# Kernel tuning notes

Hardware: AMD Instinct MI355X
Metric: run time of the kernel (lower is better)

## Reference

```python
import jax, jax.numpy as jnp
import numpy as np

B, P, N, E = 32, 1024, 1024, 128
HQ = 128  # head_num * qkv_dim == embedding_dim
SQRT_E = 11.313708498984761
LOGIT_CLIP = 10.0


def setup_inputs() -> dict:
    key = jax.random.key(0)
    ks = jax.random.split(key, 16)
    s = 1.0 / np.sqrt(E)
    return {
        "encoded_nodes": jax.random.normal(ks[0], (B, N, E), jnp.float32),
        "encoded_q1": jax.random.normal(ks[1], (B, P, E), jnp.float32),
        "encoded_q2": jax.random.normal(ks[2], (B, P, E), jnp.float32),
        "encoded_last_node": jax.random.normal(ks[3], (B, P, E), jnp.float32),
        "load": jax.random.uniform(ks[4], (B, P), jnp.float32),
        "left": jax.random.uniform(ks[5], (B, P), jnp.float32),
        "cur_dist": jax.random.uniform(ks[6], (B, P, N), jnp.float32),
        "log_scale": jnp.ones((), jnp.float32),
        "ninf_mask": jnp.zeros((B, P, N), jnp.float32),
        "Wq1": jax.random.normal(ks[7], (E, HQ), jnp.float32) * s,
        "Wq2": jax.random.normal(ks[8], (E, HQ), jnp.float32) * s,
        "Wq_last": jax.random.normal(ks[9], (E + 2, HQ), jnp.float32) * s,
        "Wk": jax.random.normal(ks[10], (E, HQ), jnp.float32) * s,
        "Wv": jax.random.normal(ks[11], (E, HQ), jnp.float32) * s,
        "AFT_dist_alpha": jnp.ones((1,), jnp.float32),
        "probs_dist_alpha": jnp.ones((1,), jnp.float32),
    }


def reference(encoded_nodes, encoded_q1, encoded_q2, encoded_last_node, load, left,
              cur_dist, log_scale, ninf_mask, Wq1, Wq2, Wq_last, Wk, Wv,
              AFT_dist_alpha, probs_dist_alpha):
    # set_kv / set_q1 / set_q2
    k = encoded_nodes @ Wk                      # [B,N,HQ]
    v = encoded_nodes @ Wv                      # [B,N,HQ]
    single_head_key = jnp.swapaxes(encoded_nodes, 1, 2)  # [B,E,N]
    q1 = encoded_q1 @ Wq1                       # [B,P,HQ]
    q2 = encoded_q2 @ Wq2

    input_cat = jnp.concatenate([encoded_last_node, load[:, :, None], left[:, :, None]], axis=2)
    q_last = input_cat @ Wq_last                # [B,P,HQ]
    q = q1 + q2 + q_last

    cur_dist_out = -cur_dist                    # [B,P,N]
    sigmoid_q = jax.nn.sigmoid(q)
    bias_scale = log_scale * AFT_dist_alpha[0] * cur_dist_out + ninf_mask
    e_bias = jnp.exp(bias_scale)                # [B,P,N]
    ek = jnp.exp(k)                             # [B,N,HQ]
    num = jnp.nan_to_num(jnp.einsum('bpn,bnd->bpd', e_bias, ek * v))
    den = jnp.nan_to_num(jnp.einsum('bpn,bnd->bpd', e_bias, ek)) + 1e-20
    AFT_out = sigmoid_q * (num / den)           # [B,P,HQ]

    score = jnp.einsum('bpd,bdn->bpn', AFT_out, single_head_key)
    score_scaled = score / SQRT_E + log_scale * probs_dist_alpha[0] * cur_dist_out
    score_clipped = LOGIT_CLIP * jnp.tanh(score_scaled)
    probs = jax.nn.softmax(score_clipped + ninf_mask, axis=2)
    return probs
```

## Files before the change

### kernel.cpp

```cpp
#include <hip/hip_runtime.h>
#include <math.h>

#define Bb 32
#define Pp 1024
#define Nn 1024

typedef unsigned short u16;
typedef __bf16 bf16x8 __attribute__((ext_vector_type(8)));
typedef float f32x4 __attribute__((ext_vector_type(4)));
typedef u16 us8 __attribute__((ext_vector_type(8)));
typedef u16 us4 __attribute__((ext_vector_type(4)));

#define MFMA __builtin_amdgcn_mfma_f32_16x16x32_bf16

static constexpr float INV_SQRT_E = 0.08838834764831845f;

__device__ __forceinline__ bf16x8 asbf(us8 v) { return __builtin_bit_cast(bf16x8, v); }

__device__ __forceinline__ void bsplit(float x, u16& h, u16& l) {
  unsigned u = __float_as_uint(x);
  unsigned r = u + 0x7FFF + ((u >> 16) & 1);
  h = (u16)(r >> 16);
  float hf = __uint_as_float((unsigned)h << 16);
  float lof = x - hf;
  unsigned u2 = __float_as_uint(lof);
  unsigned r2 = u2 + 0x7FFF + ((u2 >> 16) & 1);
  l = (u16)(r2 >> 16);
}

__device__ __forceinline__ void tsplit(float x, u16& h, u16& l) {
  unsigned u = __float_as_uint(x);
  h = (u16)(u >> 16);
  float lof = x - __uint_as_float(u & 0xFFFF0000u);
  l = (u16)(__float_as_uint(lof) >> 16);
}

__device__ __forceinline__ float exp10tanh(float s) {
  float ax = fabsf(s);
  float u = __expf(-2.0f * ax);
  float r = __builtin_amdgcn_rcpf(1.0f + u);
  float tt = fmaf(-2.0f * u, r, 1.0f);
  tt = copysignf(tt, s);
  return __expf(10.0f * tt);
}

__global__ __launch_bounds__(256) void prep_weights(
    const float* __restrict__ Wq1, const float* __restrict__ Wq2,
    const float* __restrict__ Wql, const float* __restrict__ Wk,
    const float* __restrict__ Wv, u16* __restrict__ wcat_hi, u16* __restrict__ wcat_lo,
    u16* __restrict__ wkv_hi, u16* __restrict__ wkv_lo) {
  int t = threadIdx.x;
  if (blockIdx.x == 0) {
    for (int i = t; i < 128 * 384; i += 256) {
      int c = i / 384, k = i % 384;
      float v = (k < 128) ? Wq1[k * 128 + c]
                          : (k < 256) ? Wq2[(k - 128) * 128 + c] : Wql[(k - 256) * 128 + c];
      u16 h, l;
      bsplit(v, h, l);
      wcat_hi[i] = h;
      wcat_lo[i] = l;
    }
  } else {
    for (int i = t; i < 256 * 128; i += 256) {
      int c = i >> 7, k = i & 127;
      float v = (c < 128) ? Wk[k * 128 + c] : Wv[k * 128 + (c - 128)];
      u16 h, l;
      bsplit(v, h, l);
      wkv_hi[i] = h;
      wkv_lo[i] = l;
    }
  }
}

__global__ __launch_bounds__(256, 1) void kv_prep(
    const float* __restrict__ nodes, const u16* __restrict__ wkv_hi,
    const u16* __restrict__ wkv_lo, u16* __restrict__ ekkP_hi, u16* __restrict__ ekkP_lo,
    u16* __restrict__ nodesP_hi, u16* __restrict__ nodesP_lo) {
  __shared__ u16 a_hi[32 * 136], a_lo[32 * 136];
  __shared__ float kvbuf[32 * 264];
  const int t = threadIdx.x;
  const int xcd = blockIdx.x & 7, jj = blockIdx.x >> 3;
  const int b = xcd * 4 + (jj >> 5);
  const int n0 = (jj & 31) * 32;
  for (int i = t; i < 4096; i += 256) {
    int n = i >> 7, d = i & 127;
    float v = nodes[((long)(b * 1024 + n0 + n)) * 128 + d];
    u16 h, l;
    bsplit(v, h, l);
    a_hi[n * 136 + d] = h;
    a_lo[n * 136 + d] = l;
  }
  __syncthreads();
  const int lane = t & 63, w = t >> 6;
  const int lr = lane & 15, lg = lane >> 4;
  f32x4 acc0[2][4] = {}, acc1[2][4] = {};
#pragma unroll
  for (int ks = 0; ks < 4; ++ks) {
    us8 ah[2], al[2];
#pragma unroll
    for (int mt = 0; mt < 2; ++mt) {
      int ro = (lr + 16 * mt) * 136 + ks * 32 + lg * 8;
      ah[mt] = *(const us8*)&a_hi[ro];
      al[mt] = *(const us8*)&a_lo[ro];
    }
    us8 bh[4], bl[4];
#pragma unroll
    for (int cc = 0; cc < 4; ++cc) {
      long off = (long)((w * 4 + cc) * 16 + lr) * 128 + ks * 32 + lg * 8;
      bh[cc] = *(const us8*)&wkv_hi[off];
      bl[cc] = *(const us8*)&wkv_lo[off];
    }
#pragma unroll
    for (int mt = 0; mt < 2; ++mt)
#pragma unroll
      for (int cc = 0; cc < 4; ++cc) {
        acc0[mt][cc] = MFMA(asbf(ah[mt]), asbf(bh[cc]), acc0[mt][cc], 0, 0, 0);
        acc1[mt][cc] = MFMA(asbf(al[mt]), asbf(bh[cc]), acc1[mt][cc], 0, 0, 0);
        acc1[mt][cc] = MFMA(asbf(ah[mt]), asbf(bl[cc]), acc1[mt][cc], 0, 0, 0);
      }
  }
#pragma unroll
  for (int mt = 0; mt < 2; ++mt)
#pragma unroll
    for (int cc = 0; cc < 4; ++cc) {
      int c = (w * 4 + cc) * 16 + lr;
#pragma unroll
      for (int r = 0; r < 4; ++r)
        kvbuf[(lg * 4 + r + 16 * mt) * 264 + c] = acc0[mt][cc][r] + acc1[mt][cc][r];
    }
  __syncthreads();
#pragma unroll
  for (int jo = 0; jo < 4; ++jo) {
    int c = jo * 64 + (t & 63);
    int i4 = t >> 6;
    int kcol = (c < 128) ? c : (c - 128);
    us8 h8, l8;
#pragma unroll
    for (int jq = 0; jq < 8; ++jq) {
      int n = i4 * 8 + jq;
      float kv = kvbuf[n * 264 + kcol];
      float ek = __expf(kv);
      float val = (c < 128) ? ek * kvbuf[n * 264 + c + 128] : ek;
      u16 h, l;
      bsplit(val, h, l);
      h8[jq] = h;
      l8[jq] = l;
    }
    long o = (((long)b * 128 + (n0 >> 3) + i4) * 256 + c) * 8;
    *(us8*)&ekkP_hi[o] = h8;
    *(us8*)&ekkP_lo[o] = l8;
  }
  {
    int pl = t >> 7, r = t & 127;
    int dgrp = r >> 3, nb = r & 7;
    const u16* src = pl ? a_lo : a_hi;
    u16* dst = pl ? nodesP_lo : nodesP_hi;
#pragma unroll
    for (int i = 0; i < 4; ++i) {
      int n = nb + 8 * i;
      us8 v = *(const us8*)&src[n * 136 + dgrp * 8];
      *(us8*)&dst[(((long)(b * 16 + dgrp)) * 1024 + n0 + n) * 8] = v;
    }
  }
}

__global__ __launch_bounds__(256) void qsig_prep(
    const float* __restrict__ q1m, const float* __restrict__ q2m,
    const float* __restrict__ lnm, const float* __restrict__ loadv,
    const float* __restrict__ leftv, const float* __restrict__ Wql,
    const u16* __restrict__ wcat_hi, const u16* __restrict__ wcat_lo,
    float* __restrict__ qsig) {
  const int t = threadIdx.x;
  const int lane = t & 63, w = t >> 6;
  const int lr = lane & 15, lg = lane >> 4;
  const long p0 = (long)blockIdx.x * 16;
  const long arow = p0 + lr;
  f32x4 qacc[2] = {};
#pragma unroll 2
  for (int s = 0; s < 12; ++s) {
    const float* __restrict__ src = (s < 4) ? q1m : (s < 8) ? q2m : lnm;
    long ao = arow * 128 + (s & 3) * 32 + lg * 8;
    float4 a0 = *(const float4*)&src[ao];
    float4 a1 = *(const float4*)&src[ao + 4];
    float av[8] = {a0.x, a0.y, a0.z, a0.w, a1.x, a1.y, a1.z, a1.w};
    us8 ah, al;
#pragma unroll
    for (int jq = 0; jq < 8; ++jq) {
      u16 hh, ll;
      tsplit(av[jq], hh, ll);
      ah[jq] = hh;
      al[jq] = ll;
    }
#pragma unroll
    for (int cf = 0; cf < 2; ++cf) {
      int c = w * 32 + cf * 16 + lr;
      us8 bh = *(const us8*)&wcat_hi[c * 384 + s * 32 + lg * 8];
      us8 bl = *(const us8*)&wcat_lo[c * 384 + s * 32 + lg * 8];
      qacc[cf] = MFMA(asbf(ah), asbf(bh), qacc[cf], 0, 0, 0);
      qacc[cf] = MFMA(asbf(al), asbf(bh), qacc[cf], 0, 0, 0);
      qacc[cf] = MFMA(asbf(ah), asbf(bl), qacc[cf], 0, 0, 0);
    }
  }
#pragma unroll
  for (int cf = 0; cf < 2; ++cf) {
    int c = w * 32 + cf * 16 + lr;
    float wl1 = Wql[128 * 128 + c], wl2 = Wql[129 * 128 + c];
#pragma unroll
    for (int r = 0; r < 4; ++r) {
      int row = lg * 4 + r;
      float qv = qacc[cf][r] + loadv[p0 + row] * wl1 + leftv[p0 + row] * wl2;
      qsig[(p0 + row) * 128 + c] = 1.0f / (1.0f + __expf(-qv));
    }
  }
}

struct DFset {
  float4 d0, d1, f0, f1;
};

__global__ __launch_bounds__(512, 2) void ndaft_gemm(
    const float* __restrict__ cdist, const float* __restrict__ ninf,
    const u16* __restrict__ ekkP_hi, const u16* __restrict__ ekkP_lo,
    const float* __restrict__ qsig, u16* __restrict__ aftP_hi,
    u16* __restrict__ aftP_lo, u16* __restrict__ bias16,
    const float* __restrict__ logs, const float* __restrict__ aal,
    const float* __restrict__ pal) {
  __shared__ u16 lds[25088];
  const int t = threadIdx.x;
  const int lane = t & 63, w = t >> 6;
  const int lr = lane & 15, lg = lane >> 4;
  const int wr = w >> 2, wc = w & 3;
  const int xcd = blockIdx.x & 7, j = blockIdx.x >> 3;
  const int b = xcd * 4 + (j & 3);
  const int pt = j >> 2;
  const long bp = (long)b * Pp + pt * 128;
  const float c1 = logs[0] * aal[0];
  const float c2 = logs[0] * pal[0];

  const int srow = t >> 2, soct = t & 3;
  const long arow = bp + srow;
  const long tbase = (arow >> 4) * 32768;
  const int spr = srow & 15, sptile = srow >> 4;
  const long bsrc = (long)b * 128 * 2048;

  DFset dfA, dfB;
  us8 bst[4];
  us8 ebh, ebl;

  auto load_df = [&](DFset& df, int s) {
    long ao = arow * 1024 + s * 32 + soct * 8;
    df.d0 = *(const float4*)&cdist[ao];
    df.d1 = *(const float4*)&cdist[ao + 4];
    df.f0 = *(const float4*)&ninf[ao];
    df.f1 = *(const float4*)&ninf[ao + 4];
  };
  auto load_bst = [&](int s) {
    long sb = bsrc + (long)s * 8192;
#pragma unroll
    for (int i = 0; i < 2; ++i) {
      bst[i] = *(const us8*)&ekkP_hi[sb + (i * 512 + t) * 8];
      bst[i + 2] = *(const us8*)&ekkP_lo[sb + (i * 512 + t) * 8];
    }
  };
  auto compute_eb = [&](DFset& df, int s) {
    float dv[8] = {df.d0.x, df.d0.y, df.d0.z, df.d0.w, df.d1.x, df.d1.y, df.d1.z, df.d1.w};
    float nv[8] = {df.f0.x, df.f0.y, df.f0.z, df.f0.w, df.f1.x, df.f1.y, df.f1.z, df.f1.w};
    us8 q8;
#pragma unroll
    for (int jq = 0; jq < 8; ++jq) {
      float e = __expf(fmaf(-c1, dv[jq], nv[jq]));
      u16 h, l;
      tsplit(e, h, l);
      ebh[jq] = h;
      ebl[jq] = l;
      float x = fminf(fmaxf(c2 * dv[jq], 0.f), 15.999f);
      q8[jq] = (nv[jq] < -1e5f) ? (u16)0xFFFF : (u16)(x * 4096.f + 0.5f);
    }
    *(us8*)&bias16[tbase + ((s * 4 + soct) * 16 + spr) * 8] = q8;
  };
  auto write_lds = [&]() {
    *(us8*)&lds[((sptile * 2 + 0) * 4 + soct) * 136 + spr * 8] = ebh;
    *(us8*)&lds[((sptile * 2 + 1) * 4 + soct) * 136 + spr * 8] = ebl;
#pragma unroll
    for (int i = 0; i < 2; ++i) {
      *(us8*)&lds[8704 + (i * 512 + t) * 8] = bst[i];
      *(us8*)&lds[8704 + 8192 + (i * 512 + t) * 8] = bst[i + 2];
    }
  };

  f32x4 acc[4][4] = {};

  load_df(dfA, 0);
  load_df(dfB, 1);
  load_bst(0);
  compute_eb(dfA, 0);

  auto stage = [&](int s, DFset& refill, DFset& consume) {
    asm volatile("s_waitcnt lgkmcnt(0)" ::: "memory");
    __builtin_amdgcn_s_barrier();
    __builtin_amdgcn_sched_barrier(0);
    write_lds();
    asm volatile("s_waitcnt lgkmcnt(0)" ::: "memory");
    __builtin_amdgcn_s_barrier();
    __builtin_amdgcn_sched_barrier(0);
    if (s < 31) load_bst(s + 1);
    if (s < 30) load_df(refill, s + 2);
    if (s < 31) compute_eb(consume, s + 1);
    us8 ah[4], al[4];
#pragma unroll
    for (int mt = 0; mt < 4; ++mt) {
      int ptl = wr * 4 + mt;
      ah[mt] = *(const us8*)&lds[((ptl * 2 + 0) * 4 + lg) * 136 + lr * 8];
      al[mt] = *(const us8*)&lds[((ptl * 2 + 1) * 4 + lg) * 136 + lr * 8];
    }
#pragma unroll
    for (int ct = 0; ct < 4; ++ct) {
      int c = (ct < 2) ? (wc * 32 + ct * 16 + lr) : (96 + wc * 32 + ct * 16 + lr);
      us8 bh = *(const us8*)&lds[8704 + lg * 2048 + c * 8];
      us8 bl = *(const us8*)&lds[8704 + 8192 + lg * 2048 + c * 8];
#pragma unroll
      for (int mt = 0; mt < 4; ++mt) {
        acc[mt][ct] = MFMA(asbf(ah[mt]), asbf(bh), acc[mt][ct], 0, 0, 0);
        acc[mt][ct] = MFMA(asbf(al[mt]), asbf(bh), acc[mt][ct], 0, 0, 0);
        acc[mt][ct] = MFMA(asbf(ah[mt]), asbf(bl), acc[mt][ct], 0, 0, 0);
      }
    }
  };

#pragma unroll 1
  for (int s2 = 0; s2 < 32; s2 += 2) {
    stage(s2, dfA, dfB);
    stage(s2 + 1, dfB, dfA);
  }

#pragma unroll
  for (int mt = 0; mt < 4; ++mt)
#pragma unroll
    for (int ct = 0; ct < 2; ++ct) {
      int cn = wc * 32 + ct * 16 + lr;
      int nc = cn >> 3, jq = cn & 7;
#pragma unroll
      for (int r = 0; r < 4; ++r) {
        long gr = bp + wr * 64 + mt * 16 + lg * 4 + r;
        float sig = qsig[gr * 128 + cn];
        float aftv = sig * acc[mt][ct][r] * __builtin_amdgcn_rcpf(acc[mt][ct + 2][r] + 1e-20f);
        u16 h, l;
        bsplit(aftv, h, l);
        long idx = (gr >> 4) * 2048 + (nc * 16 + (gr & 15)) * 8 + jq;
        aftP_hi[idx] = h;
        aftP_lo[idx] = l;
      }
    }
}

__global__ __launch_bounds__(256, 4) void score_softmax(
    const u16* bias16, const u16* __restrict__ aftP_hi, const u16* __restrict__ aftP_lo,
    const u16* __restrict__ nodesP_hi, const u16* __restrict__ nodesP_lo,
    float* out) {
  __shared__ float psum[16 * 4];
  __shared__ float invb[16];
  const int t = threadIdx.x;
  const int lane = t & 63, w = t >> 6;
  const int lr = lane & 15, lg = lane >> 4;
  const int xcd = blockIdx.x & 7, j = blockIdx.x >> 3;
  const int b = xcd * 4 + (j >> 6);
  const int tl = j & 63;
  const int p0 = tl * 16;
  const long bp = (long)b * Pp + p0;
  const int tile = b * 64 + tl;

  f32x4 sacc[16] = {};
#pragma unroll
  for (int ks = 0; ks < 4; ++ks) {
    long aoff = (long)tile * 2048 + ((long)((ks * 4 + lg) * 16 + lr)) * 8;
    us8 ah = *(const us8*)&aftP_hi[aoff];
    us8 al = *(const us8*)&aftP_lo[aoff];
    long nb = ((long)(b * 16 + ks * 4 + lg)) * 1024;
    auto bld = [&](int cf, us8& bh, us8& bl) {
      long o = (nb + w * 256 + cf * 16 + lr) * 8;
      bh = *(const us8*)&nodesP_hi[o];
      bl = *(const us8*)&nodesP_lo[o];
    };
    us8 bh0, bl0, bh1, bl1;
    bld(0, bh0, bl0);
    bld(1, bh1, bl1);
#pragma unroll
    for (int cf = 0; cf < 16; ++cf) {
      us8 nh = bh1, nl = bl1;
      if (cf < 14) bld(cf + 2, nh, nl);
      sacc[cf] = MFMA(asbf(bh0), asbf(ah), sacc[cf], 0, 0, 0);
      sacc[cf] = MFMA(asbf(bl0), asbf(ah), sacc[cf], 0, 0, 0);
      sacc[cf] = MFMA(asbf(bh0), asbf(al), sacc[cf], 0, 0, 0);
      bh0 = bh1; bl0 = bl1; bh1 = nh; bl1 = nl;
    }
  }

  const long btile = (long)tile * 32768;
  float rs = 0.f;
#pragma unroll
  for (int cf = 0; cf < 16; ++cf) {
    int nc = w * 32 + cf * 2 + (lg >> 1);
    int j0 = (lg & 1) * 4;
    us4 q4 = *(const us4*)&bias16[btile + (nc * 16 + lr) * 8 + j0];
#pragma unroll
    for (int r = 0; r < 4; ++r) {
      u16 qv = q4[r];
      float sv = fmaf(sacc[cf][r], INV_SQRT_E, (float)qv * -2.44140625e-4f);
      float e = exp10tanh(sv);
      e = (qv == (u16)0xFFFF) ? 0.f : e;
      sacc[cf][r] = e;
      rs += e;
    }
  }
  rs += __shfl_xor(rs, 16);
  rs += __shfl_xor(rs, 32);
  if (lane < 16) psum[lr * 4 + w] = rs;
  __syncthreads();
  if (t < 16)
    invb[t] = 1.0f / (psum[t * 4] + psum[t * 4 + 1] + psum[t * 4 + 2] + psum[t * 4 + 3]);
  __syncthreads();

  const float inv = invb[lr];
  const long ro = (bp + lr) * (long)Nn + w * 256;
#pragma unroll
  for (int cf = 0; cf < 16; ++cf) {
    float4 v;
    v.x = sacc[cf][0] * inv;
    v.y = sacc[cf][1] * inv;
    v.z = sacc[cf][2] * inv;
    v.w = sacc[cf][3] * inv;
    *(float4*)&out[ro + cf * 16 + lg * 4] = v;
  }
}

extern "C" void kernel_launch(void* const* d_in, const int* in_sizes, int n_in,
                              void* d_out, int out_size, void* d_ws, size_t ws_size,
                              hipStream_t stream) {
  const float* nodes = (const float*)d_in[0];
  const float* q1m = (const float*)d_in[1];
  const float* q2m = (const float*)d_in[2];
  const float* lnm = (const float*)d_in[3];
  const float* loadv = (const float*)d_in[4];
  const float* leftv = (const float*)d_in[5];
  const float* cdist = (const float*)d_in[6];
  const float* logs = (const float*)d_in[7];
  const float* ninf = (const float*)d_in[8];
  const float* Wq1 = (const float*)d_in[9];
  const float* Wq2 = (const float*)d_in[10];
  const float* Wql = (const float*)d_in[11];
  const float* Wk = (const float*)d_in[12];
  const float* Wv = (const float*)d_in[13];
  const float* aalpha = (const float*)d_in[14];
  const float* palpha = (const float*)d_in[15];

  char* ws = (char*)d_ws;
  u16* ekkP_hi = (u16*)ws;
  u16* ekkP_lo = (u16*)(ws + (16ul << 20));
  u16* nodesP_hi = (u16*)(ws + (32ul << 20));
  u16* nodesP_lo = (u16*)(ws + (40ul << 20));
  float* qsig = (float*)(ws + (48ul << 20));
  u16* aftP_hi = (u16*)(ws + (64ul << 20));
  u16* aftP_lo = (u16*)(ws + (72ul << 20));
  u16* wcat_hi = (u16*)(ws + (80ul << 20));
  u16* wcat_lo = wcat_hi + 128 * 384;
  u16* wkv_hi = wcat_lo + 128 * 384;
  u16* wkv_lo = wkv_hi + 256 * 128;
  u16* bias16 = (u16*)d_out;

  prep_weights<<<2, 256, 0, stream>>>(Wq1, Wq2, Wql, Wk, Wv, wcat_hi, wcat_lo, wkv_hi, wkv_lo);
  kv_prep<<<Bb * Nn / 32, 256, 0, stream>>>(nodes, wkv_hi, wkv_lo, ekkP_hi, ekkP_lo,
                                            nodesP_hi, nodesP_lo);
  qsig_prep<<<2048, 256, 0, stream>>>(q1m, q2m, lnm, loadv, leftv, Wql, wcat_hi, wcat_lo,
                                      qsig);
  ndaft_gemm<<<256, 512, 0, stream>>>(cdist, ninf, ekkP_hi, ekkP_lo, qsig, aftP_hi,
                                      aftP_lo, bias16, logs, aalpha, palpha);
  score_softmax<<<Bb * Pp / 16, 256, 0, stream>>>(
      bias16, aftP_hi, aftP_lo, nodesP_hi, nodesP_lo, (float*)d_out);
}
```

Baseline: 349.3 us.

## Load B operand directly to registers and double-buffer A tile in LDS

The ek/ekv B-operand fragments are now loaded straight from global memory into registers in MFMA layout, instead of being staged through LDS. The A tile (exp bias split into hi/lo) is double-buffered in LDS, which drops one of the two barriers per k-step. The aim is less LDS traffic and less barrier stalling in the main GEMM loop. The cost is more VGPRs for two sets of B registers and redundant global reads of B, since each wave fetches its own columns.

New measurement: 359.9 us. +3.0%, slower.

```diff
diff --git a/kernel.cpp b/kernel.cpp
--- a/kernel.cpp
+++ b/kernel.cpp
@@ -225,7 +225,7 @@
     u16* __restrict__ aftP_lo, u16* __restrict__ bias16,
     const float* __restrict__ logs, const float* __restrict__ aal,
     const float* __restrict__ pal) {
-  __shared__ u16 lds[25088];
+  __shared__ u16 lds[2][8704];
   const int t = threadIdx.x;
   const int lane = t & 63, w = t >> 6;
   const int lr = lane & 15, lg = lane >> 4;
@@ -243,8 +243,12 @@
   const int spr = srow & 15, sptile = srow >> 4;
   const long bsrc = (long)b * 128 * 2048;
 
+  int ccol[4];
+#pragma unroll
+  for (int ct = 0; ct < 4; ++ct)
+    ccol[ct] = (ct < 2) ? (wc * 32 + ct * 16 + lr) : (96 + wc * 32 + ct * 16 + lr);
+
   DFset dfA, dfB;
-  us8 bst[4];
   us8 ebh, ebl;
 
   auto load_df = [&](DFset& df, int s) {
@@ -254,12 +258,12 @@
     df.f0 = *(const float4*)&ninf[ao];
     df.f1 = *(const float4*)&ninf[ao + 4];
   };
-  auto load_bst = [&](int s) {
-    long sb = bsrc + (long)s * 8192;
-#pragma unroll
-    for (int i = 0; i < 2; ++i) {
-      bst[i] = *(const us8*)&ekkP_hi[sb + (i * 512 + t) * 8];
-      bst[i + 2] = *(const us8*)&ekkP_lo[sb + (i * 512 + t) * 8];
+  auto load_B = [&](int s, us8 (&bh)[4], us8 (&bl)[4]) {
+    long sb = bsrc + (long)s * 8192 + (long)lg * 2048;
+#pragma unroll
+    for (int ct = 0; ct < 4; ++ct) {
+      bh[ct] = *(const us8*)&ekkP_hi[sb + ccol[ct] * 8];
+      bl[ct] = *(const us8*)&ekkP_lo[sb + ccol[ct] * 8];
     }
   };
   auto compute_eb = [&](DFset& df, int s) {
@@ -278,59 +282,57 @@
     }
     *(us8*)&bias16[tbase + ((s * 4 + soct) * 16 + spr) * 8] = q8;
   };
-  auto write_lds = [&]() {
-    *(us8*)&lds[((sptile * 2 + 0) * 4 + soct) * 136 + spr * 8] = ebh;
-    *(us8*)&lds[((sptile * 2 + 1) * 4 + soct) * 136 + spr * 8] = ebl;
-#pragma unroll
-    for (int i = 0; i < 2; ++i) {
-      *(us8*)&lds[8704 + (i * 512 + t) * 8] = bst[i];
-      *(us8*)&lds[8704 + 8192 + (i * 512 + t) * 8] = bst[i + 2];
-    }
+  auto write_A = [&](int buf) {
+    *(us8*)&lds[buf][((sptile * 2 + 0) * 4 + soct) * 136 + spr * 8] = ebh;
+    *(us8*)&lds[buf][((sptile * 2 + 1) * 4 + soct) * 136 + spr * 8] = ebl;
   };
 
   f32x4 acc[4][4] = {};
+  us8 Bh0[4], Bl0[4], Bh1[4], Bl1[4];
 
   load_df(dfA, 0);
   load_df(dfB, 1);
-  load_bst(0);
+  load_B(0, Bh0, Bl0);
   compute_eb(dfA, 0);
-
-  auto stage = [&](int s, DFset& refill, DFset& consume) {
+  write_A(0);
+  asm volatile("s_waitcnt lgkmcnt(0)" ::: "memory");
+  __builtin_amdgcn_s_barrier();
+  __builtin_amdgcn_sched_barrier(0);
+
+  auto stage = [&](int s, DFset& refill, DFset& consume, us8 (&BhC)[4], us8 (&BlC)[4],
+                   us8 (&BhN)[4], us8 (&BlN)[4]) {
+    if (s < 31) load_B(s + 1, BhN, BlN);
+    if (s < 30) load_df(refill, s + 2);
+    if (s < 31) {
+      compute_eb(consume, s + 1);
+      write_A((s + 1) & 1);
+    }
+    const int buf = s & 1;
+    us8 ah[4], al[4];
+#pragma unroll
+    for (int mt = 0; mt < 4; ++mt) {
+      int ptl = wr * 4 + mt;
+      ah[mt] = *(const us8*)&lds[buf][((ptl * 2 + 0) * 4 + lg) * 136 + lr * 8];
+      al[mt] = *(const us8*)&lds[buf][((ptl * 2 + 1) * 4 + lg) * 136 + lr * 8];
+    }
+#pragma unroll
+    for (int ct = 0; ct < 4; ++ct) {
+#pragma unroll
+      for (int mt = 0; mt < 4; ++mt) {
+        acc[mt][ct] = MFMA(asbf(ah[mt]), asbf(BhC[ct]), acc[mt][ct], 0, 0, 0);
+        acc[mt][ct] = MFMA(asbf(al[mt]), asbf(BhC[ct]), acc[mt][ct], 0, 0, 0);
+        acc[mt][ct] = MFMA(asbf(ah[mt]), asbf(BlC[ct]), acc[mt][ct], 0, 0, 0);
+      }
+    }
     asm volatile("s_waitcnt lgkmcnt(0)" ::: "memory");
     __builtin_amdgcn_s_barrier();
     __builtin_amdgcn_sched_barrier(0);
-    write_lds();
-    asm volatile("s_waitcnt lgkmcnt(0)" ::: "memory");
-    __builtin_amdgcn_s_barrier();
-    __builtin_amdgcn_sched_barrier(0);
-    if (s < 31) load_bst(s + 1);
-    if (s < 30) load_df(refill, s + 2);
-    if (s < 31) compute_eb(consume, s + 1);
-    us8 ah[4], al[4];
-#pragma unroll
-    for (int mt = 0; mt < 4; ++mt) {
-      int ptl = wr * 4 + mt;
-      ah[mt] = *(const us8*)&lds[((ptl * 2 + 0) * 4 + lg) * 136 + lr * 8];
-      al[mt] = *(const us8*)&lds[((ptl * 2 + 1) * 4 + lg) * 136 + lr * 8];
-    }
-#pragma unroll
-    for (int ct = 0; ct < 4; ++ct) {
-      int c = (ct < 2) ? (wc * 32 + ct * 16 + lr) : (96 + wc * 32 + ct * 16 + lr);
-      us8 bh = *(const us8*)&lds[8704 + lg * 2048 + c * 8];
-      us8 bl = *(const us8*)&lds[8704 + 8192 + lg * 2048 + c * 8];
-#pragma unroll
-      for (int mt = 0; mt < 4; ++mt) {
-        acc[mt][ct] = MFMA(asbf(ah[mt]), asbf(bh), acc[mt][ct], 0, 0, 0);
-        acc[mt][ct] = MFMA(asbf(al[mt]), asbf(bh), acc[mt][ct], 0, 0, 0);
-        acc[mt][ct] = MFMA(asbf(ah[mt]), asbf(bl), acc[mt][ct], 0, 0, 0);
-      }
-    }
   };
 
 #pragma unroll 1
   for (int s2 = 0; s2 < 32; s2 += 2) {
-    stage(s2, dfA, dfB);
-    stage(s2 + 1, dfB, dfA);
+    stage(s2, dfA, dfB, Bh0, Bl0, Bh1, Bl1);
+    stage(s2 + 1, dfB, dfA, Bh1, Bl1, Bh0, Bl0);
   }
 
 #pragma unroll
```

## Load B panel via direct global-to-LDS DMA and coalesce bias16 stores with shuffles

Applied to the files above, without the earlier changes.

The ekk B panel is now moved straight from global memory into LDS with global_load_lds instead of being staged through registers. This frees VGPRs and removes the register-to-LDS write step. The bias16 quantized output is transposed across lanes with shuffles so that each wave writes a contiguous 1 KB chunk. The main loop is also simplified to a single stage per iteration with plain __syncthreads, which drops the earlier software prefetch of B one stage ahead, so the DMA latency is now exposed within each stage.

Result: slower. 455.8 us (+30.5%).

```diff
diff --git a/kernel.cpp b/kernel.cpp
--- a/kernel.cpp
+++ b/kernel.cpp
@@ -42,6 +42,12 @@
   float tt = fmaf(-2.0f * u, r, 1.0f);
   tt = copysignf(tt, s);
   return __expf(10.0f * tt);
+}
+
+__device__ __forceinline__ void dma16(const void* g, char* lds_dst) {
+  __builtin_amdgcn_global_load_lds(
+      (const __attribute__((address_space(1))) unsigned*)g,
+      (__attribute__((address_space(3))) unsigned*)lds_dst, 16, 0, 0);
 }
 
 __global__ __launch_bounds__(256) void prep_weights(
@@ -218,6 +224,10 @@
   float4 d0, d1, f0, f1;
 };
 
+#define A_OFF 0
+#define BHI_OFF 17408
+#define BLO_OFF 33792
+
 __global__ __launch_bounds__(512, 2) void ndaft_gemm(
     const float* __restrict__ cdist, const float* __restrict__ ninf,
     const u16* __restrict__ ekkP_hi, const u16* __restrict__ ekkP_lo,
@@ -225,7 +235,8 @@
     u16* __restrict__ aftP_lo, u16* __restrict__ bias16,
     const float* __restrict__ logs, const float* __restrict__ aal,
     const float* __restrict__ pal) {
-  __shared__ u16 lds[25088];
+  __shared__ __align__(16) char smem[50176];
+  u16* Albs = (u16*)smem;
   const int t = threadIdx.x;
   const int lane = t & 63, w = t >> 6;
   const int lr = lane & 15, lg = lane >> 4;
@@ -239,13 +250,12 @@
 
   const int srow = t >> 2, soct = t & 3;
   const long arow = bp + srow;
-  const long tbase = (arow >> 4) * 32768;
-  const int spr = srow & 15, sptile = srow >> 4;
-  const long bsrc = (long)b * 128 * 2048;
+  const long wtile_u16 = ((bp >> 4) + w) * 32768;
+  const long bpanel_bytes = (long)b * 262144 * 2;
 
   DFset dfA, dfB;
-  us8 bst[4];
   us8 ebh, ebl;
+  unsigned qd[4];
 
   auto load_df = [&](DFset& df, int s) {
     long ao = arow * 1024 + s * 32 + soct * 8;
@@ -254,15 +264,7 @@
     df.f0 = *(const float4*)&ninf[ao];
     df.f1 = *(const float4*)&ninf[ao + 4];
   };
-  auto load_bst = [&](int s) {
-    long sb = bsrc + (long)s * 8192;
-#pragma unroll
-    for (int i = 0; i < 2; ++i) {
-      bst[i] = *(const us8*)&ekkP_hi[sb + (i * 512 + t) * 8];
-      bst[i + 2] = *(const us8*)&ekkP_lo[sb + (i * 512 + t) * 8];
-    }
-  };
-  auto compute_eb = [&](DFset& df, int s) {
+  auto compute_eb = [&](DFset& df) {
     float dv[8] = {df.d0.x, df.d0.y, df.d0.z, df.d0.w, df.d1.x, df.d1.y, df.d1.z, df.d1.w};
     float nv[8] = {df.f0.x, df.f0.y, df.f0.z, df.f0.w, df.f1.x, df.f1.y, df.f1.z, df.f1.w};
     us8 q8;
@@ -276,48 +278,71 @@
       float x = fminf(fmaxf(c2 * dv[jq], 0.f), 15.999f);
       q8[jq] = (nv[jq] < -1e5f) ? (u16)0xFFFF : (u16)(x * 4096.f + 0.5f);
     }
-    *(us8*)&bias16[tbase + ((s * 4 + soct) * 16 + spr) * 8] = q8;
+    unsigned raw[4];
+#pragma unroll
+    for (int k2 = 0; k2 < 4; ++k2) raw[k2] = ((const unsigned*)&q8)[k2];
+    int srcl = (lane & 15) * 4 + (lane >> 4);
+#pragma unroll
+    for (int k2 = 0; k2 < 4; ++k2) qd[k2] = __shfl(raw[k2], srcl);
   };
-  auto write_lds = [&]() {
-    *(us8*)&lds[((sptile * 2 + 0) * 4 + soct) * 136 + spr * 8] = ebh;
-    *(us8*)&lds[((sptile * 2 + 1) * 4 + soct) * 136 + spr * 8] = ebl;
+  auto store_bias = [&](int s) {
+    us8 qp;
+#pragma unroll
+    for (int k2 = 0; k2 < 4; ++k2) ((unsigned*)&qp)[k2] = qd[k2];
+    *(us8*)&bias16[wtile_u16 + (long)s * 512 + lane * 8] = qp;
+  };
+  auto write_A = [&]() {
+    int spr = srow & 15, sptile = srow >> 4;
+    *(us8*)&Albs[((sptile * 2 + 0) * 4 + soct) * 136 + spr * 8] = ebh;
+    *(us8*)&Albs[((sptile * 2 + 1) * 4 + soct) * 136 + spr * 8] = ebl;
+  };
+  auto dma_B = [&](int s) {
+    long sbytes = bpanel_bytes + (long)s * 16384;
 #pragma unroll
     for (int i = 0; i < 2; ++i) {
-      *(us8*)&lds[8704 + (i * 512 + t) * 8] = bst[i];
-      *(us8*)&lds[8704 + 8192 + (i * 512 + t) * 8] = bst[i + 2];
+      int c2 = w * 2 + i;
+      long so = sbytes + (long)c2 * 1024 + (long)lane * 16;
+      dma16((const char*)ekkP_hi + so, smem + BHI_OFF + c2 * 1024);
+      dma16((const char*)ekkP_lo + so, smem + BLO_OFF + c2 * 1024);
     }
   };
+
+  int ccol[4];
+#pragma unroll
+  for (int ct = 0; ct < 4; ++ct)
+    ccol[ct] = ((ct < 2) ? (wc * 32 + ct * 16) : (96 + wc * 32 + ct * 16)) + lr;
 
   f32x4 acc[4][4] = {};
 
   load_df(dfA, 0);
   load_df(dfB, 1);
-  load_bst(0);
-  compute_eb(dfA, 0);
-
-  auto stage = [&](int s, DFset& refill, DFset& consume) {
-    asm volatile("s_waitcnt lgkmcnt(0)" ::: "memory");
-    __builtin_amdgcn_s_barrier();
-    __builtin_amdgcn_sched_barrier(0);
-    write_lds();
-    asm volatile("s_waitcnt lgkmcnt(0)" ::: "memory");
-    __builtin_amdgcn_s_barrier();
-    __builtin_amdgcn_sched_barrier(0);
-    if (s < 31) load_bst(s + 1);
+  compute_eb(dfA);
+  store_bias(0);
+
+#pragma unroll 1
+  for (int s = 0; s < 32; ++s) {
+    __syncthreads();
+    write_A();
+    dma_B(s);
+    DFset& refill = (s & 1) ? dfB : dfA;
+    DFset& consume = (s & 1) ? dfA : dfB;
     if (s < 30) load_df(refill, s + 2);
-    if (s < 31) compute_eb(consume, s + 1);
+    if (s < 31) {
+      compute_eb(consume);
+      store_bias(s + 1);
+    }
+    __syncthreads();
     us8 ah[4], al[4];
 #pragma unroll
     for (int mt = 0; mt < 4; ++mt) {
       int ptl = wr * 4 + mt;
-      ah[mt] = *(const us8*)&lds[((ptl * 2 + 0) * 4 + lg) * 136 + lr * 8];
-      al[mt] = *(const us8*)&lds[((ptl * 2 + 1) * 4 + lg) * 136 + lr * 8];
+      ah[mt] = *(const us8*)&Albs[((ptl * 2 + 0) * 4 + lg) * 136 + lr * 8];
+      al[mt] = *(const us8*)&Albs[((ptl * 2 + 1) * 4 + lg) * 136 + lr * 8];
     }
 #pragma unroll
     for (int ct = 0; ct < 4; ++ct) {
-      int c = (ct < 2) ? (wc * 32 + ct * 16 + lr) : (96 + wc * 32 + ct * 16 + lr);
-      us8 bh = *(const us8*)&lds[8704 + lg * 2048 + c * 8];
-      us8 bl = *(const us8*)&lds[8704 + 8192 + lg * 2048 + c * 8];
+      us8 bh = *(const us8*)(smem + BHI_OFF + (lg * 256 + ccol[ct]) * 16);
+      us8 bl = *(const us8*)(smem + BLO_OFF + (lg * 256 + ccol[ct]) * 16);
 #pragma unroll
       for (int mt = 0; mt < 4; ++mt) {
         acc[mt][ct] = MFMA(asbf(ah[mt]), asbf(bh), acc[mt][ct], 0, 0, 0);
@@ -325,12 +350,6 @@
         acc[mt][ct] = MFMA(asbf(ah[mt]), asbf(bl), acc[mt][ct], 0, 0, 0);
       }
     }
-  };
-
-#pragma unroll 1
-  for (int s2 = 0; s2 < 32; s2 += 2) {
-    stage(s2, dfA, dfB);
-    stage(s2 + 1, dfB, dfA);
   }
 
 #pragma unroll
```
